# Kernel tuning notes

Measured on AMD Instinct MI355X. Metric: run time of the kernel, lower is better.

The kernel has to match this reference:

```python
import jax, jax.numpy as jnp
import numpy as np

N_EMBD = 1024
N_HEAD = 16
HEAD_DIM = 64


def setup_inputs() -> dict:
    key = jax.random.key(0)
    ks = jax.random.split(key, 5)
    x = jax.random.normal(ks[0], (4, 2048, N_EMBD), dtype=jnp.float32)
    # qkv_proj: Linear(n_embd, 3*n_embd) -- torch weight is [out, in]
    W_qkv = jax.random.normal(ks[1], (3 * N_EMBD, N_EMBD), dtype=jnp.float32) * 0.02
    b_qkv = jnp.zeros((3 * N_EMBD,), dtype=jnp.float32)
    W_out = jax.random.normal(ks[2], (N_EMBD, N_EMBD), dtype=jnp.float32) * 0.02
    b_out = jnp.zeros((N_EMBD,), dtype=jnp.float32)
    return {"x": x, "W_qkv": W_qkv, "b_qkv": b_qkv, "W_out": W_out, "b_out": b_out}


def reference(x, W_qkv, b_qkv, W_out, b_out):
    B, S, C = x.shape
    scale = 1.0 / np.sqrt(HEAD_DIM)
    qkv = jnp.einsum('bsc,oc->bso', x, W_qkv) + b_qkv  # [B,S,3C]
    q, k, v = jnp.split(qkv, 3, axis=-1)
    # [B,S,C] -> [B,H,S,Dh]
    def to_heads(t):
        return t.reshape(B, S, N_HEAD, HEAD_DIM).transpose(0, 2, 1, 3)
    q, k, v = to_heads(q), to_heads(k), to_heads(v)
    scores = jnp.einsum('bhqd,bhkd->bhqk', q, k) * scale  # [B,H,S,S]
    causal = jnp.tril(jnp.ones((S, S), dtype=bool))
    scores = jnp.where(causal[None, None], scores, -jnp.inf)
    weights = jax.nn.softmax(scores.astype(jnp.float32), axis=-1).astype(q.dtype)
    y = jnp.einsum('bhqk,bhkd->bhqd', weights, v)  # [B,H,S,Dh]
    y = y.transpose(0, 2, 1, 3).reshape(B, S, C)
    return jnp.einsum('bsc,oc->bso', y, W_out) + b_out
```

## Files before the change

### kernel.cpp

```cpp
#include <hip/hip_runtime.h>
#include <stdint.h>
#include <stddef.h>

typedef __attribute__((ext_vector_type(8))) short short8;
typedef __attribute__((ext_vector_type(4))) float f32x4;
typedef __attribute__((ext_vector_type(16))) float f32x16;
typedef __attribute__((ext_vector_type(4))) unsigned short ushort4v;
typedef __attribute__((ext_vector_type(4))) unsigned int uint4v;

#define SEQ   2048
#define NH    16
#define BATCH 4
#define GK    1024

__device__ __forceinline__ unsigned short f2bf(float f) {
  union { float f; unsigned int u; } v; v.f = f;
  unsigned int u = v.u;
  u += 0x7fffu + ((u >> 16) & 1u);
  return (unsigned short)(u >> 16);
}

__device__ __forceinline__ unsigned cvtpk_bf16(float lo, float hi) {
  unsigned r;
  asm("v_cvt_pk_bf16_f32 %0, %1, %2" : "=v"(r) : "v"(lo), "v"(hi));
  return r;
}

__device__ __forceinline__ void plswap(unsigned &x, unsigned &y) {
#if __has_builtin(__builtin_amdgcn_permlane32_swap)
  auto r = __builtin_amdgcn_permlane32_swap((int)x, (int)y, false, false);
  x = (unsigned)r[0]; y = (unsigned)r[1];
#else
  const unsigned sx = (unsigned)__shfl_xor((int)x, 32);
  const unsigned sy = (unsigned)__shfl_xor((int)y, 32);
  const bool hi = (threadIdx.x & 63) >= 32;
  const unsigned nx = hi ? sy : x;
  const unsigned ny = hi ? y : sx;
  x = nx; y = ny;
#endif
}

__device__ __forceinline__ void gload16(const unsigned short* g, unsigned short* l) {
  __builtin_amdgcn_global_load_lds(
      (const __attribute__((address_space(1))) unsigned int*)g,
      (__attribute__((address_space(3))) unsigned int*)l, 16, 0, 0);
}

__global__ void cvt_bf16(const float* __restrict__ src, unsigned short* __restrict__ dst, int n4) {
  int i = blockIdx.x * blockDim.x + threadIdx.x;
  const int stride = gridDim.x * blockDim.x;
  for (; i < n4; i += stride) {
    const float4 v = reinterpret_cast<const float4*>(src)[i];
    ushort4v o;
    o[0] = f2bf(v.x); o[1] = f2bf(v.y); o[2] = f2bf(v.z); o[3] = f2bf(v.w);
    reinterpret_cast<ushort4v*>(dst)[i] = o;
  }
}

template<int MODE>
__global__ __launch_bounds__(256, 2)
void gemm_bt(const unsigned short* __restrict__ A,
             const unsigned short* __restrict__ Bw,
             const float* __restrict__ bias,
             unsigned short* __restrict__ q_ws,
             unsigned short* __restrict__ k_ws,
             unsigned short* __restrict__ v_ws,
             float* __restrict__ fout,
             int N)
{
  __shared__ __attribute__((aligned(16))) unsigned short As[128 * 64];
  __shared__ __attribute__((aligned(16))) unsigned short Bs[128 * 64];

  const int t = threadIdx.x;
  const int w = t >> 6, lane = t & 63;
  const int g = lane >> 4, c = lane & 15;
  const int wrow = w >> 1, wcol = w & 1;
  const int m0 = blockIdx.y * 128;
  const int n0 = blockIdx.x * 128;

  const int r8 = lane >> 3;
  const int cgs = (lane & 7) ^ r8;

  const f32x4 fz = {0.f, 0.f, 0.f, 0.f};
  f32x4 acc[4][4];
#pragma unroll
  for (int i = 0; i < 4; ++i)
#pragma unroll
    for (int j = 0; j < 4; ++j) acc[i][j] = fz;

  for (int ks = 0; ks < GK; ks += 64) {
    __syncthreads();
#pragma unroll
    for (int i = 0; i < 4; ++i) {
      const int RB = (i * 4 + w) * 8;
      gload16(A + (size_t)(m0 + RB + r8) * GK + ks + cgs * 8, &As[RB * 64]);
      gload16(Bw + (size_t)(n0 + RB + r8) * GK + ks + cgs * 8, &Bs[RB * 64]);
    }
    __syncthreads();
#pragma unroll
    for (int kk = 0; kk < 2; ++kk) {
      short8 af[4], bfr[4];
#pragma unroll
      for (int mi = 0; mi < 4; ++mi) {
        const int row = wrow * 64 + mi * 16 + c;
        af[mi] = *reinterpret_cast<const short8*>(&As[row * 64 + (((kk * 4 + g) ^ (row & 7)) << 3)]);
      }
#pragma unroll
      for (int ni = 0; ni < 4; ++ni) {
        const int row = wcol * 64 + ni * 16 + c;
        bfr[ni] = *reinterpret_cast<const short8*>(&Bs[row * 64 + (((kk * 4 + g) ^ (row & 7)) << 3)]);
      }
#pragma unroll
      for (int mi = 0; mi < 4; ++mi)
#pragma unroll
        for (int ni = 0; ni < 4; ++ni)
          acc[mi][ni] = __builtin_amdgcn_mfma_f32_16x16x32_bf16(af[mi], bfr[ni], acc[mi][ni], 0, 0, 0);
    }
  }

  if (MODE == 0) {
    const int sec = n0 >> 10;
    unsigned short* dst = (sec == 0) ? q_ws : ((sec == 1) ? k_ws : v_ws);
    const float qsc = (sec == 0) ? (0.125f * 1.44269504f) : 1.0f;
#pragma unroll
    for (int ni = 0; ni < 4; ++ni) {
      const int n = n0 + wcol * 64 + ni * 16 + c;
      const float bb = bias[n];
      const int hh = (n & 1023) >> 6;
      const int d = n & 63;
#pragma unroll
      for (int mi = 0; mi < 4; ++mi) {
#pragma unroll
        for (int r = 0; r < 4; ++r) {
          const int m = m0 + wrow * 64 + mi * 16 + g * 4 + r;
          const int b = m >> 11, s = m & 2047;
          const float val = (acc[mi][ni][r] + bb) * qsc;
          dst[((size_t)((b * NH + hh) * SEQ + s) << 6) + d] = f2bf(val);
        }
      }
    }
  } else {
#pragma unroll
    for (int ni = 0; ni < 4; ++ni) {
      const int n = n0 + wcol * 64 + ni * 16 + c;
      const float bb = bias[n];
#pragma unroll
      for (int mi = 0; mi < 4; ++mi) {
#pragma unroll
        for (int r = 0; r < 4; ++r) {
          const int m = m0 + wrow * 64 + mi * 16 + g * 4 + r;
          fout[(size_t)m * N + n] = acc[mi][ni][r] + bb;
        }
      }
    }
  }
}

__global__ __launch_bounds__(256)
void transpose_v(const unsigned short* __restrict__ v, unsigned short* __restrict__ vt) {
  __shared__ unsigned short T[64][72];
  const int t = threadIdx.x;
  const int bh = blockIdx.y, s0 = blockIdx.x * 64;
  const unsigned short* src = v + ((size_t)bh * SEQ + s0) * 64;
#pragma unroll
  for (int rep = 0; rep < 2; ++rep) {
    const int u = rep * 256 + t;
    const int sr = u >> 3, cg = u & 7;
    const short8 x = *reinterpret_cast<const short8*>(src + (size_t)sr * 64 + cg * 8);
    *reinterpret_cast<short8*>(&T[sr][cg * 8]) = x;
  }
  __syncthreads();
  unsigned short* dst = vt + (size_t)bh * 64 * SEQ + s0;
#pragma unroll
  for (int rep = 0; rep < 2; ++rep) {
    const int u = rep * 256 + t;
    const int d = u >> 3, sc8 = u & 7;
    short8 x;
#pragma unroll
    for (int j = 0; j < 8; ++j) x[j] = (short)T[sc8 * 8 + j][d];
    *reinterpret_cast<short8*>(dst + (size_t)d * SEQ + sc8 * 8) = x;
  }
}

__global__ __launch_bounds__(256, 2)
void attn_fwd3(const unsigned short* __restrict__ q_ws,
               const unsigned short* __restrict__ k_ws,
               const unsigned short* __restrict__ vt_ws,
               unsigned short* __restrict__ y_ws)
{
  __shared__ __attribute__((aligned(16))) unsigned short Ks[2][64 * 64];
  __shared__ __attribute__((aligned(16))) unsigned short Vs[2][64 * 64];

  const int t = threadIdx.x;
  const int w = t >> 6, lane = t & 63;
  const int ql = lane & 31, hi = lane >> 5;
  const int bh = blockIdx.y, b = bh >> 4, h = bh & 15;

  const int s_row = t >> 3, s_cg = t & 7;
  const int so0 = s_row * 64 + ((s_cg ^ (s_row & 7)) << 3);
  const int so1 = (s_row + 32) * 64 + ((s_cg ^ (s_row & 7)) << 3);

  const unsigned short* kbase = k_ws + (size_t)bh * SEQ * 64;
  const unsigned short* vbase = vt_ws + (size_t)bh * 64 * SEQ;

  short8 rk0, rk1, rv0, rv1;
  auto stage_issue = [&](int kt) {
    const unsigned short* kp = kbase + (size_t)kt * 64 * 64;
    rk0 = *reinterpret_cast<const short8*>(kp + (size_t)s_row * 64 + s_cg * 8);
    rk1 = *reinterpret_cast<const short8*>(kp + (size_t)(s_row + 32) * 64 + s_cg * 8);
    const unsigned short* vp = vbase + kt * 64;
    rv0 = *reinterpret_cast<const short8*>(vp + (size_t)s_row * SEQ + s_cg * 8);
    rv1 = *reinterpret_cast<const short8*>(vp + (size_t)(s_row + 32) * SEQ + s_cg * 8);
  };
  auto stage_write = [&](int bi) {
    *reinterpret_cast<short8*>(&Ks[bi][so0]) = rk0;
    *reinterpret_cast<short8*>(&Ks[bi][so1]) = rk1;
    *reinterpret_cast<short8*>(&Vs[bi][so0]) = rv0;
    *reinterpret_cast<short8*>(&Vs[bi][so1]) = rv1;
  };

#pragma unroll 1
  for (int pi = 0; pi < 2; ++pi) {
    const int jt = pi ? (7 - blockIdx.x) : blockIdx.x;
    const int wq0 = jt * 256 + w * 64;
    const int nkt = 4 * jt + 4;

    const unsigned short* qrA = q_ws + ((size_t)bh * SEQ + (wq0 + ql)) * 64;
    const unsigned short* qrB = qrA + 32 * 64;
    short8 qfA[4], qfB[4];
#pragma unroll
    for (int ks = 0; ks < 4; ++ks) {
      qfA[ks] = *reinterpret_cast<const short8*>(qrA + ks * 16 + hi * 8);
      qfB[ks] = *reinterpret_cast<const short8*>(qrB + ks * 16 + hi * 8);
    }

    f32x16 oA0, oA1, oB0, oB1;
#pragma unroll
    for (int i = 0; i < 16; ++i) { oA0[i] = 0.f; oA1[i] = 0.f; oB0[i] = 0.f; oB1[i] = 0.f; }
    float mA = -1e30f, lA = 0.f, mB = -1e30f, lB = 0.f;

    stage_issue(0);
    stage_write(0);

    auto softmax_pack = [&](f32x16& s0, f32x16& s1, float& m_run, float& lsum,
                            f32x16& o0, f32x16& o1, short8* pa) {
      float tm = -1e30f;
#pragma unroll
      for (int r = 0; r < 16; ++r) tm = fmaxf(tm, fmaxf(s0[r], s1[r]));
      tm = fmaxf(tm, __shfl_xor(tm, 32));
      if (__any(tm > m_run + 10.0f)) {
        const float m_new = fmaxf(m_run, tm);
        const float al = __builtin_amdgcn_exp2f(m_run - m_new);
        m_run = m_new;
        lsum *= al;
#pragma unroll
        for (int r = 0; r < 16; ++r) {
          const int qq = (r & 3) + 8 * (r >> 2) + 4 * hi;
          const float ar = __shfl(al, qq);
          o0[r] *= ar; o1[r] *= ar;
        }
      }
      float psum = 0.f;
      unsigned W[16];
#pragma unroll
      for (int half = 0; half < 2; ++half) {
#pragma unroll
        for (int gr = 0; gr < 4; ++gr) {
          const float v0 = (half ? s1[gr * 4 + 0] : s0[gr * 4 + 0]) - m_run;
          const float v1 = (half ? s1[gr * 4 + 1] : s0[gr * 4 + 1]) - m_run;
          const float v2 = (half ? s1[gr * 4 + 2] : s0[gr * 4 + 2]) - m_run;
          const float v3 = (half ? s1[gr * 4 + 3] : s0[gr * 4 + 3]) - m_run;
          const float p0 = __builtin_amdgcn_exp2f(v0);
          const float p1 = __builtin_amdgcn_exp2f(v1);
          const float p2 = __builtin_amdgcn_exp2f(v2);
          const float p3 = __builtin_amdgcn_exp2f(v3);
          psum += (p0 + p1) + (p2 + p3);
          W[half * 8 + 2 * gr]     = cvtpk_bf16(p0, p1);
          W[half * 8 + 2 * gr + 1] = cvtpk_bf16(p2, p3);
        }
      }
      lsum += psum;
#pragma unroll
      for (int q4 = 0; q4 < 4; ++q4) {
        unsigned a0 = W[q4 * 4 + 0], a1 = W[q4 * 4 + 2];
        unsigned b0 = W[q4 * 4 + 1], b1 = W[q4 * 4 + 3];
        plswap(a0, a1);
        plswap(b0, b1);
        uint4v pk; pk[0] = a0; pk[1] = b0; pk[2] = a1; pk[3] = b1;
        pa[q4] = __builtin_bit_cast(short8, pk);
      }
    };

#pragma unroll 1
    for (int kt = 0; kt < nkt; ++kt) {
      const bool more = (kt + 1) < nkt;
      if (more) stage_issue(kt + 1);
      __syncthreads();
      const int cur = kt & 1;
      const int kt64 = kt * 64;

      if (kt64 <= wq0 + 63) {
        short8 kfl[4], kfh[4];
#pragma unroll
        for (int ks = 0; ks < 4; ++ks) {
          kfl[ks] = *reinterpret_cast<const short8*>(
              &Ks[cur][ql * 64 + (((2 * ks + hi) ^ (ql & 7)) << 3)]);
          kfh[ks] = *reinterpret_cast<const short8*>(
              &Ks[cur][(32 + ql) * 64 + (((2 * ks + hi) ^ (ql & 7)) << 3)]);
        }
        const bool actA = kt64 <= wq0 + 31;
        short8 paA[4], paB[4];

        if (actA) {
          f32x16 s0, s1;
#pragma unroll
          for (int i = 0; i < 16; ++i) { s0[i] = 0.f; s1[i] = 0.f; }
#pragma unroll
          for (int ks = 0; ks < 4; ++ks) {
            s0 = __builtin_amdgcn_mfma_f32_32x32x16_bf16(kfl[ks], qfA[ks], s0, 0, 0, 0);
            s1 = __builtin_amdgcn_mfma_f32_32x32x16_bf16(kfh[ks], qfA[ks], s1, 0, 0, 0);
          }
          if (kt64 + 63 > wq0) {
            const int gq = wq0 + ql;
#pragma unroll
            for (int r = 0; r < 16; ++r) {
              const int krow = (r & 3) + 8 * (r >> 2) + 4 * hi;
              if (kt64 + krow > gq)      s0[r] = -1e30f;
              if (kt64 + 32 + krow > gq) s1[r] = -1e30f;
            }
          }
          softmax_pack(s0, s1, mA, lA, oA0, oA1, paA);
        }
        {
          f32x16 s0, s1;
#pragma unroll
          for (int i = 0; i < 16; ++i) { s0[i] = 0.f; s1[i] = 0.f; }
#pragma unroll
          for (int ks = 0; ks < 4; ++ks) {
            s0 = __builtin_amdgcn_mfma_f32_32x32x16_bf16(kfl[ks], qfB[ks], s0, 0, 0, 0);
            s1 = __builtin_amdgcn_mfma_f32_32x32x16_bf16(kfh[ks], qfB[ks], s1, 0, 0, 0);
          }
          if (kt64 + 63 > wq0 + 32) {
            const int gq = wq0 + 32 + ql;
#pragma unroll
            for (int r = 0; r < 16; ++r) {
              const int krow = (r & 3) + 8 * (r >> 2) + 4 * hi;
              if (kt64 + krow > gq)      s0[r] = -1e30f;
              if (kt64 + 32 + krow > gq) s1[r] = -1e30f;
            }
          }
          softmax_pack(s0, s1, mB, lB, oB0, oB1, paB);
        }
#pragma unroll
        for (int ks = 0; ks < 4; ++ks) {
          const short8 vfl = *reinterpret_cast<const short8*>(
              &Vs[cur][ql * 64 + (((2 * ks + hi) ^ (ql & 7)) << 3)]);
          const short8 vfh = *reinterpret_cast<const short8*>(
              &Vs[cur][(32 + ql) * 64 + (((2 * ks + hi) ^ (ql & 7)) << 3)]);
          oB0 = __builtin_amdgcn_mfma_f32_32x32x16_bf16(paB[ks], vfl, oB0, 0, 0, 0);
          oB1 = __builtin_amdgcn_mfma_f32_32x32x16_bf16(paB[ks], vfh, oB1, 0, 0, 0);
          if (actA) {
            oA0 = __builtin_amdgcn_mfma_f32_32x32x16_bf16(paA[ks], vfl, oA0, 0, 0, 0);
            oA1 = __builtin_amdgcn_mfma_f32_32x32x16_bf16(paA[ks], vfh, oA1, 0, 0, 0);
          }
        }
      }
      if (more) stage_write((kt + 1) & 1);
    }

    auto fin = [&](f32x16& o0, f32x16& o1, float lsum, int qbase) {
      lsum += __shfl_xor(lsum, 32);
      const float linv = 1.f / lsum;
#pragma unroll
      for (int r = 0; r < 16; ++r) {
        const int qq = (r & 3) + 8 * (r >> 2) + 4 * hi;
        const float lr = __shfl(linv, qq);
        const size_t rowo = ((size_t)b * SEQ + (qbase + qq)) * 1024 + h * 64;
        y_ws[rowo + ql]      = f2bf(o0[r] * lr);
        y_ws[rowo + 32 + ql] = f2bf(o1[r] * lr);
      }
    };
    fin(oA0, oA1, lA, wq0);
    fin(oB0, oB1, lB, wq0 + 32);
    __syncthreads();
  }
}

extern "C" void kernel_launch(void* const* d_in, const int* in_sizes, int n_in,
                              void* d_out, int out_size, void* d_ws, size_t ws_size,
                              hipStream_t stream)
{
  (void)in_sizes; (void)n_in; (void)out_size; (void)ws_size;
  const float* x     = (const float*)d_in[0];
  const float* W_qkv = (const float*)d_in[1];
  const float* b_qkv = (const float*)d_in[2];
  const float* W_out = (const float*)d_in[3];
  const float* b_out = (const float*)d_in[4];
  float* out = (float*)d_out;

  unsigned short* ws      = (unsigned short*)d_ws;
  unsigned short* x_bf    = ws;
  unsigned short* wqkv_bf = x_bf    + (size_t)8192 * 1024;
  unsigned short* wout_bf = wqkv_bf + (size_t)3072 * 1024;
  unsigned short* q_ws    = wout_bf + (size_t)1024 * 1024;
  unsigned short* k_ws    = q_ws    + (size_t)64 * SEQ * 64;
  unsigned short* v_ws    = k_ws    + (size_t)64 * SEQ * 64;
  unsigned short* y_ws    = v_ws    + (size_t)64 * SEQ * 64;
  unsigned short* vt_ws   = x_bf;

  cvt_bf16<<<2048, 256, 0, stream>>>(x,     x_bf,    (8192 * 1024) / 4);
  cvt_bf16<<<1024, 256, 0, stream>>>(W_qkv, wqkv_bf, (3072 * 1024) / 4);
  cvt_bf16<<<512,  256, 0, stream>>>(W_out, wout_bf, (1024 * 1024) / 4);

  gemm_bt<0><<<dim3(24, 64), 256, 0, stream>>>(x_bf, wqkv_bf, b_qkv, q_ws, k_ws, v_ws, nullptr, 3072);
  transpose_v<<<dim3(SEQ / 64, 64), 256, 0, stream>>>(v_ws, vt_ws);
  attn_fwd3<<<dim3(4, 64), 256, 0, stream>>>(q_ws, k_ws, vt_ws, y_ws);
  gemm_bt<1><<<dim3(8, 64), 256, 0, stream>>>(y_ws, wout_bf, b_out, nullptr, nullptr, nullptr, out, 1024);
}
```

Baseline: 193.6 us.

## Split attention into 8-wave blocks with one 32-query tile per wave

The attention kernel is restructured so that each 512-thread block handles one 256-query tile. Each of its 8 waves owns 32 queries, replacing the old scheme where 4 waves each processed two 32-query groups across two paired tiles. Load balance across causal tiles now comes from reversing the tile order for the upper half of the batch-head grid. MFMA sections are wrapped in s_setprio. The aim is more concurrent waves and blocks to hide latency, in exchange for less reuse of K/V loaded into LDS per wave and tighter register budgets.

After: 180.9 us. -6.6%, faster.

```diff
diff --git a/kernel.cpp b/kernel.cpp
--- a/kernel.cpp
+++ b/kernel.cpp
@@ -182,8 +182,8 @@
   }
 }
 
-__global__ __launch_bounds__(256, 2)
-void attn_fwd3(const unsigned short* __restrict__ q_ws,
+__global__ __launch_bounds__(512, 4)
+void attn_fwd4(const unsigned short* __restrict__ q_ws,
                const unsigned short* __restrict__ k_ws,
                const unsigned short* __restrict__ vt_ws,
                unsigned short* __restrict__ y_ws)
@@ -195,55 +195,76 @@
   const int w = t >> 6, lane = t & 63;
   const int ql = lane & 31, hi = lane >> 5;
   const int bh = blockIdx.y, b = bh >> 4, h = bh & 15;
+  const int jt = (blockIdx.y >= 32) ? (7 - (int)blockIdx.x) : (int)blockIdx.x;
+  const int wq0 = jt * 256 + w * 32;
+  const int nkt = 4 * jt + 4;
 
   const int s_row = t >> 3, s_cg = t & 7;
-  const int so0 = s_row * 64 + ((s_cg ^ (s_row & 7)) << 3);
-  const int so1 = (s_row + 32) * 64 + ((s_cg ^ (s_row & 7)) << 3);
+  const int so = s_row * 64 + ((s_cg ^ (s_row & 7)) << 3);
 
   const unsigned short* kbase = k_ws + (size_t)bh * SEQ * 64;
   const unsigned short* vbase = vt_ws + (size_t)bh * 64 * SEQ;
 
-  short8 rk0, rk1, rv0, rv1;
+  short8 rk, rv;
   auto stage_issue = [&](int kt) {
-    const unsigned short* kp = kbase + (size_t)kt * 64 * 64;
-    rk0 = *reinterpret_cast<const short8*>(kp + (size_t)s_row * 64 + s_cg * 8);
-    rk1 = *reinterpret_cast<const short8*>(kp + (size_t)(s_row + 32) * 64 + s_cg * 8);
-    const unsigned short* vp = vbase + kt * 64;
-    rv0 = *reinterpret_cast<const short8*>(vp + (size_t)s_row * SEQ + s_cg * 8);
-    rv1 = *reinterpret_cast<const short8*>(vp + (size_t)(s_row + 32) * SEQ + s_cg * 8);
+    rk = *reinterpret_cast<const short8*>(kbase + (size_t)kt * 4096 + s_row * 64 + s_cg * 8);
+    rv = *reinterpret_cast<const short8*>(vbase + (size_t)s_row * SEQ + kt * 64 + s_cg * 8);
   };
   auto stage_write = [&](int bi) {
-    *reinterpret_cast<short8*>(&Ks[bi][so0]) = rk0;
-    *reinterpret_cast<short8*>(&Ks[bi][so1]) = rk1;
-    *reinterpret_cast<short8*>(&Vs[bi][so0]) = rv0;
-    *reinterpret_cast<short8*>(&Vs[bi][so1]) = rv1;
+    *reinterpret_cast<short8*>(&Ks[bi][so]) = rk;
+    *reinterpret_cast<short8*>(&Vs[bi][so]) = rv;
   };
 
+  const unsigned short* qr = q_ws + ((size_t)bh * SEQ + (wq0 + ql)) * 64;
+  short8 qf[4];
+#pragma unroll
+  for (int ks = 0; ks < 4; ++ks)
+    qf[ks] = *reinterpret_cast<const short8*>(qr + ks * 16 + hi * 8);
+
+  f32x16 o0, o1;
+#pragma unroll
+  for (int i = 0; i < 16; ++i) { o0[i] = 0.f; o1[i] = 0.f; }
+  float m_run = -1e30f, lsum = 0.f;
+
+  stage_issue(0);
+  stage_write(0);
+
 #pragma unroll 1
-  for (int pi = 0; pi < 2; ++pi) {
-    const int jt = pi ? (7 - blockIdx.x) : blockIdx.x;
-    const int wq0 = jt * 256 + w * 64;
-    const int nkt = 4 * jt + 4;
-
-    const unsigned short* qrA = q_ws + ((size_t)bh * SEQ + (wq0 + ql)) * 64;
-    const unsigned short* qrB = qrA + 32 * 64;
-    short8 qfA[4], qfB[4];
-#pragma unroll
-    for (int ks = 0; ks < 4; ++ks) {
-      qfA[ks] = *reinterpret_cast<const short8*>(qrA + ks * 16 + hi * 8);
-      qfB[ks] = *reinterpret_cast<const short8*>(qrB + ks * 16 + hi * 8);
-    }
-
-    f32x16 oA0, oA1, oB0, oB1;
-#pragma unroll
-    for (int i = 0; i < 16; ++i) { oA0[i] = 0.f; oA1[i] = 0.f; oB0[i] = 0.f; oB1[i] = 0.f; }
-    float mA = -1e30f, lA = 0.f, mB = -1e30f, lB = 0.f;
-
-    stage_issue(0);
-    stage_write(0);
-
-    auto softmax_pack = [&](f32x16& s0, f32x16& s1, float& m_run, float& lsum,
-                            f32x16& o0, f32x16& o1, short8* pa) {
+  for (int kt = 0; kt < nkt; ++kt) {
+    const bool more = (kt + 1) < nkt;
+    if (more) stage_issue(kt + 1);
+    __syncthreads();
+    const int cur = kt & 1;
+    const int kt64 = kt * 64;
+
+    if (kt64 <= wq0 + 31) {
+      short8 kfl[4], kfh[4];
+#pragma unroll
+      for (int ks = 0; ks < 4; ++ks) {
+        kfl[ks] = *reinterpret_cast<const short8*>(
+            &Ks[cur][ql * 64 + (((2 * ks + hi) ^ (ql & 7)) << 3)]);
+        kfh[ks] = *reinterpret_cast<const short8*>(
+            &Ks[cur][(32 + ql) * 64 + (((2 * ks + hi) ^ (ql & 7)) << 3)]);
+      }
+      f32x16 s0, s1;
+#pragma unroll
+      for (int i = 0; i < 16; ++i) { s0[i] = 0.f; s1[i] = 0.f; }
+      __builtin_amdgcn_s_setprio(1);
+#pragma unroll
+      for (int ks = 0; ks < 4; ++ks) {
+        s0 = __builtin_amdgcn_mfma_f32_32x32x16_bf16(kfl[ks], qf[ks], s0, 0, 0, 0);
+        s1 = __builtin_amdgcn_mfma_f32_32x32x16_bf16(kfh[ks], qf[ks], s1, 0, 0, 0);
+      }
+      __builtin_amdgcn_s_setprio(0);
+      if (kt64 + 63 > wq0) {
+        const int gq = wq0 + ql;
+#pragma unroll
+        for (int r = 0; r < 16; ++r) {
+          const int krow = (r & 3) + 8 * (r >> 2) + 4 * hi;
+          if (kt64 + krow > gq)      s0[r] = -1e30f;
+          if (kt64 + 32 + krow > gq) s1[r] = -1e30f;
+        }
+      }
       float tm = -1e30f;
 #pragma unroll
       for (int r = 0; r < 16; ++r) tm = fmaxf(tm, fmaxf(s0[r], s1[r]));
@@ -280,6 +301,7 @@
         }
       }
       lsum += psum;
+      short8 pa[4];
 #pragma unroll
       for (int q4 = 0; q4 < 4; ++q4) {
         unsigned a0 = W[q4 * 4 + 0], a1 = W[q4 * 4 + 2];
@@ -289,100 +311,30 @@
         uint4v pk; pk[0] = a0; pk[1] = b0; pk[2] = a1; pk[3] = b1;
         pa[q4] = __builtin_bit_cast(short8, pk);
       }
-    };
-
-#pragma unroll 1
-    for (int kt = 0; kt < nkt; ++kt) {
-      const bool more = (kt + 1) < nkt;
-      if (more) stage_issue(kt + 1);
-      __syncthreads();
-      const int cur = kt & 1;
-      const int kt64 = kt * 64;
-
-      if (kt64 <= wq0 + 63) {
-        short8 kfl[4], kfh[4];
-#pragma unroll
-        for (int ks = 0; ks < 4; ++ks) {
-          kfl[ks] = *reinterpret_cast<const short8*>(
-              &Ks[cur][ql * 64 + (((2 * ks + hi) ^ (ql & 7)) << 3)]);
-          kfh[ks] = *reinterpret_cast<const short8*>(
-              &Ks[cur][(32 + ql) * 64 + (((2 * ks + hi) ^ (ql & 7)) << 3)]);
-        }
-        const bool actA = kt64 <= wq0 + 31;
-        short8 paA[4], paB[4];
-
-        if (actA) {
-          f32x16 s0, s1;
-#pragma unroll
-          for (int i = 0; i < 16; ++i) { s0[i] = 0.f; s1[i] = 0.f; }
-#pragma unroll
-          for (int ks = 0; ks < 4; ++ks) {
-            s0 = __builtin_amdgcn_mfma_f32_32x32x16_bf16(kfl[ks], qfA[ks], s0, 0, 0, 0);
-            s1 = __builtin_amdgcn_mfma_f32_32x32x16_bf16(kfh[ks], qfA[ks], s1, 0, 0, 0);
-          }
-          if (kt64 + 63 > wq0) {
-            const int gq = wq0 + ql;
-#pragma unroll
-            for (int r = 0; r < 16; ++r) {
-              const int krow = (r & 3) + 8 * (r >> 2) + 4 * hi;
-              if (kt64 + krow > gq)      s0[r] = -1e30f;
-              if (kt64 + 32 + krow > gq) s1[r] = -1e30f;
-            }
-          }
-          softmax_pack(s0, s1, mA, lA, oA0, oA1, paA);
-        }
-        {
-          f32x16 s0, s1;
-#pragma unroll
-          for (int i = 0; i < 16; ++i) { s0[i] = 0.f; s1[i] = 0.f; }
-#pragma unroll
-          for (int ks = 0; ks < 4; ++ks) {
-            s0 = __builtin_amdgcn_mfma_f32_32x32x16_bf16(kfl[ks], qfB[ks], s0, 0, 0, 0);
-            s1 = __builtin_amdgcn_mfma_f32_32x32x16_bf16(kfh[ks], qfB[ks], s1, 0, 0, 0);
-          }
-          if (kt64 + 63 > wq0 + 32) {
-            const int gq = wq0 + 32 + ql;
-#pragma unroll
-            for (int r = 0; r < 16; ++r) {
-              const int krow = (r & 3) + 8 * (r >> 2) + 4 * hi;
-              if (kt64 + krow > gq)      s0[r] = -1e30f;
-              if (kt64 + 32 + krow > gq) s1[r] = -1e30f;
-            }
-          }
-          softmax_pack(s0, s1, mB, lB, oB0, oB1, paB);
-        }
-#pragma unroll
-        for (int ks = 0; ks < 4; ++ks) {
-          const short8 vfl = *reinterpret_cast<const short8*>(
-              &Vs[cur][ql * 64 + (((2 * ks + hi) ^ (ql & 7)) << 3)]);
-          const short8 vfh = *reinterpret_cast<const short8*>(
-              &Vs[cur][(32 + ql) * 64 + (((2 * ks + hi) ^ (ql & 7)) << 3)]);
-          oB0 = __builtin_amdgcn_mfma_f32_32x32x16_bf16(paB[ks], vfl, oB0, 0, 0, 0);
-          oB1 = __builtin_amdgcn_mfma_f32_32x32x16_bf16(paB[ks], vfh, oB1, 0, 0, 0);
-          if (actA) {
-            oA0 = __builtin_amdgcn_mfma_f32_32x32x16_bf16(paA[ks], vfl, oA0, 0, 0, 0);
-            oA1 = __builtin_amdgcn_mfma_f32_32x32x16_bf16(paA[ks], vfh, oA1, 0, 0, 0);
-          }
-        }
-      }
-      if (more) stage_write((kt + 1) & 1);
-    }
-
-    auto fin = [&](f32x16& o0, f32x16& o1, float lsum, int qbase) {
-      lsum += __shfl_xor(lsum, 32);
-      const float linv = 1.f / lsum;
-#pragma unroll
-      for (int r = 0; r < 16; ++r) {
-        const int qq = (r & 3) + 8 * (r >> 2) + 4 * hi;
-        const float lr = __shfl(linv, qq);
-        const size_t rowo = ((size_t)b * SEQ + (qbase + qq)) * 1024 + h * 64;
-        y_ws[rowo + ql]      = f2bf(o0[r] * lr);
-        y_ws[rowo + 32 + ql] = f2bf(o1[r] * lr);
-      }
-    };
-    fin(oA0, oA1, lA, wq0);
-    fin(oB0, oB1, lB, wq0 + 32);
-    __syncthreads();
+      __builtin_amdgcn_s_setprio(1);
+#pragma unroll
+      for (int ks = 0; ks < 4; ++ks) {
+        const short8 vfl = *reinterpret_cast<const short8*>(
+            &Vs[cur][ql * 64 + (((2 * ks + hi) ^ (ql & 7)) << 3)]);
+        const short8 vfh = *reinterpret_cast<const short8*>(
+            &Vs[cur][(32 + ql) * 64 + (((2 * ks + hi) ^ (ql & 7)) << 3)]);
+        o0 = __builtin_amdgcn_mfma_f32_32x32x16_bf16(pa[ks], vfl, o0, 0, 0, 0);
+        o1 = __builtin_amdgcn_mfma_f32_32x32x16_bf16(pa[ks], vfh, o1, 0, 0, 0);
+      }
+      __builtin_amdgcn_s_setprio(0);
+    }
+    if (more) stage_write((kt + 1) & 1);
+  }
+
+  lsum += __shfl_xor(lsum, 32);
+  const float linv = 1.f / lsum;
+#pragma unroll
+  for (int r = 0; r < 16; ++r) {
+    const int qq = (r & 3) + 8 * (r >> 2) + 4 * hi;
+    const float lr = __shfl(linv, qq);
+    const size_t rowo = ((size_t)b * SEQ + (wq0 + qq)) * 1024 + h * 64;
+    y_ws[rowo + ql]      = f2bf(o0[r] * lr);
+    y_ws[rowo + 32 + ql] = f2bf(o1[r] * lr);
   }
 }
 
@@ -414,6 +366,6 @@
 
   gemm_bt<0><<<dim3(24, 64), 256, 0, stream>>>(x_bf, wqkv_bf, b_qkv, q_ws, k_ws, v_ws, nullptr, 3072);
   transpose_v<<<dim3(SEQ / 64, 64), 256, 0, stream>>>(v_ws, vt_ws);
-  attn_fwd3<<<dim3(4, 64), 256, 0, stream>>>(q_ws, k_ws, vt_ws, y_ws);
+  attn_fwd4<<<dim3(8, 64), 512, 0, stream>>>(q_ws, k_ws, vt_ws, y_ws);
   gemm_bt<1><<<dim3(8, 64), 256, 0, stream>>>(y_ws, wout_bf, b_out, nullptr, nullptr, nullptr, out, 1024);
 }
```
